# Performance work log

Measured on AMD Instinct MI355X. Metric: run time of the kernel, lower is better.

The kernel has to match this reference:

```python
import jax, jax.numpy as jnp
import numpy as np

B, N, D = 2, 2048, 1024
H, HD = 16, 64
SCALE = HD ** (-0.5)


def setup_inputs() -> dict:
    key = jax.random.key(0)
    k1, k2, k3, k4 = jax.random.split(key, 4)
    x = jax.random.normal(k1, (B, N, D), dtype=jnp.float32)
    mask = jax.random.randint(k2, (B, 1, N, N), 0, 2) == 1  # bool, True = masked out
    W_qkv = jax.random.normal(k3, (D, 3 * H * HD), dtype=jnp.float32) * (D ** -0.5)
    W_out = jax.random.normal(k4, (H * HD, D), dtype=jnp.float32) * ((H * HD) ** -0.5)
    b_out = jnp.zeros((D,), dtype=jnp.float32)
    return {"x": x, "mask": mask, "W_qkv": W_qkv, "W_out": W_out, "b_out": b_out}


def reference(x, mask, W_qkv, W_out, b_out):
    b, n, _ = x.shape
    qkv = x @ W_qkv                                  # [b, n, 3*h*hd]
    q, k, v = jnp.split(qkv, 3, axis=-1)
    split_heads = lambda t: t.reshape(b, n, H, HD).transpose(0, 2, 1, 3)  # b h n d
    q, k, v = split_heads(q), split_heads(k), split_heads(v)
    scores = jnp.einsum('bhid,bhjd->bhij', q, k) * SCALE
    scores = jnp.where(mask, jnp.finfo(scores.dtype).min, scores)
    attn = jax.nn.softmax(scores, axis=-1)           # dropout p=0 -> identity
    out = jnp.einsum('bhij,bhjd->bhid', attn, v)     # [b, h, n, hd]
    out = out.transpose(0, 2, 1, 3).reshape(b, n, H * HD)
    return out @ W_out + b_out
```

## Files before the change

### kernel.cpp

```cpp
#include <hip/hip_runtime.h>
#include <stdint.h>

typedef unsigned short u16;
typedef short short8 __attribute__((ext_vector_type(8)));
typedef float f32x4 __attribute__((ext_vector_type(4)));
typedef float f32x16 __attribute__((ext_vector_type(16)));
typedef unsigned int uint2v __attribute__((ext_vector_type(2)));

#define K2E 0.18033688011112042f

__device__ __forceinline__ u16 f2bf(float f) {
  union { float f; uint32_t u; } v;
  v.f = f;
  uint32_t u = v.u;
  u += 0x7FFFu + ((u >> 16) & 1u);
  return (u16)(u >> 16);
}

__device__ __forceinline__ uint32_t cvtpk(float lo, float hi) {
  uint32_t r;
  asm("v_cvt_pk_bf16_f32 %0, %1, %2" : "=v"(r) : "v"(lo), "v"(hi));
  return r;
}

__device__ __forceinline__ float exp2a(float x) {
  float r;
  asm("v_exp_f32 %0, %1" : "=v"(r) : "v"(x));
  return r;
}

__device__ __forceinline__ float mask_zero(float p, uint32_t zm, int oc) {
  int mext = __builtin_amdgcn_sbfe((int)zm, oc, 1);
  float r;
  asm("v_bfi_b32 %0, %1, 0, %2" : "=v"(r) : "v"(mext), "v"(p));
  return r;
}

__device__ __forceinline__ void gld_lds16(const u16* src, char* dst) {
  __builtin_amdgcn_global_load_lds((const __attribute__((address_space(1))) void*)src,
                                   (__attribute__((address_space(3))) void*)dst, 16, 0, 0);
}

__device__ __forceinline__ void pack_frags(const f32x16& v, short8& fa, short8& fb) {
  union U { uint32_t w[4]; short8 v8; };
  uint32_t X0 = cvtpk(v[0], v[1]),   X1 = cvtpk(v[2], v[3]);
  uint32_t Y0 = cvtpk(v[4], v[5]),   Y1 = cvtpk(v[6], v[7]);
  uint32_t X2 = cvtpk(v[8], v[9]),   X3 = cvtpk(v[10], v[11]);
  uint32_t Y2 = cvtpk(v[12], v[13]), Y3 = cvtpk(v[14], v[15]);
  uint2v r0 = __builtin_amdgcn_permlane32_swap(X0, Y0, false, false);
  uint2v r1 = __builtin_amdgcn_permlane32_swap(X1, Y1, false, false);
  uint2v r2 = __builtin_amdgcn_permlane32_swap(X2, Y2, false, false);
  uint2v r3 = __builtin_amdgcn_permlane32_swap(X3, Y3, false, false);
  U ua; ua.w[0] = r0.x; ua.w[1] = r1.x; ua.w[2] = r0.y; ua.w[3] = r1.y; fa = ua.v8;
  U ub; ub.w[0] = r2.x; ub.w[1] = r3.x; ub.w[2] = r2.y; ub.w[3] = r3.y; fb = ub.v8;
}

__global__ __launch_bounds__(256) void k_prep(const float* __restrict__ x,
                                              u16* __restrict__ xb,
                                              const float* __restrict__ Wqkv,
                                              u16* __restrict__ wqT,
                                              const float* __restrict__ Wout,
                                              u16* __restrict__ woT,
                                              const int* __restrict__ m,
                                              uint32_t* __restrict__ mw) {
  __shared__ float tsh[32][33];
  const int bid = blockIdx.x;
  const int t = threadIdx.x;
  if (bid < 4096) {
    int g = bid * 256 + t;
    float4 v = ((const float4*)x)[g];
    ushort4 o;
    o.x = f2bf(v.x); o.y = f2bf(v.y); o.z = f2bf(v.z); o.w = f2bf(v.w);
    ((ushort4*)xb)[g] = o;
  } else if (bid < 8192) {
    const float* src; u16* dst; int R, C, bb;
    if (bid < 7168) { src = Wqkv; dst = wqT; R = 1024; C = 3072; bb = bid - 4096;
    } else           { src = Wout; dst = woT; R = 1024; C = 1024; bb = bid - 7168; }
    const int nbx = C >> 5;
    const int c0 = (bb % nbx) * 32, r0 = (bb / nbx) * 32;
    const int tx = t & 31, ty = t >> 5;
#pragma unroll
    for (int i = 0; i < 4; ++i)
      tsh[ty + 8 * i][tx] = src[(size_t)(r0 + ty + 8 * i) * C + c0 + tx];
    __syncthreads();
#pragma unroll
    for (int i = 0; i < 4; ++i)
      dst[(size_t)(c0 + ty + 8 * i) * R + r0 + tx] = f2bf(tsh[tx][ty + 8 * i]);
  } else {
    int g = (bid - 8192) * 256 + t;
    unsigned long long bal = __ballot(m[g] != 0);
    int lane = t & 63;
    if (lane == 0) mw[g >> 5] = (uint32_t)bal;
    else if (lane == 32) mw[g >> 5] = (uint32_t)(bal >> 32);
  }
}


#define GS(U, BUF)                                                   \
  {                                                                  \
    char* dA_ = lds + (BUF) * 16384 + (w << 11);                     \
    const u16* a_ = As + ((U) << 5);                                 \
    const u16* b_ = Bs + ((U) << 5);                                 \
    gld_lds16(a_, dA_);                                              \
    gld_lds16(a_ + (K << 4), dA_ + 1024);                            \
    gld_lds16(b_, dA_ + 8192);                                       \
    gld_lds16(b_ + (K << 4), dA_ + 9216);                            \
  }

#define PH(U, BUF, DOSTAGE, VMS)                                                          \
  {                                                                                       \
    asm volatile("s_waitcnt vmcnt(" VMS ")" ::: "memory");                                \
    __builtin_amdgcn_sched_barrier(0);                                                    \
    __builtin_amdgcn_s_barrier();                                                         \
    __builtin_amdgcn_sched_barrier(0);                                                    \
    const char* rb_ = lds + (BUF) * 16384;                                                \
    short8 af[4], bfr[4];                                                                 \
    _Pragma("unroll")                                                                     \
    for (int mi = 0; mi < 4; ++mi) {                                                      \
      int row = wm * 64 + mi * 16 + lr;                                                   \
      af[mi] = *(const short8*)(rb_ + row * 64 + ((lg ^ ((row >> 1) & 3)) << 4));         \
    }                                                                                     \
    _Pragma("unroll")                                                                     \
    for (int ni = 0; ni < 4; ++ni) {                                                      \
      int row = wn * 64 + ni * 16 + lr;                                                   \
      bfr[ni] = *(const short8*)(rb_ + 8192 + row * 64 + ((lg ^ ((row >> 1) & 3)) << 4)); \
    }                                                                                     \
    asm volatile("s_waitcnt lgkmcnt(0)" ::: "memory");                                    \
    __builtin_amdgcn_sched_barrier(0);                                                    \
    __builtin_amdgcn_s_barrier();                                                        \
    __builtin_amdgcn_sched_barrier(0);                                                    \
    if (DOSTAGE) GS((U) + 3, BUF);                                                        \
    __builtin_amdgcn_s_setprio(1);                                                        \
    _Pragma("unroll")                                                                     \
    for (int mi = 0; mi < 4; ++mi)                                                        \
      _Pragma("unroll")                                                                   \
      for (int ni = 0; ni < 4; ++ni)                                                      \
        acc[mi][ni] =                                                                     \
            __builtin_amdgcn_mfma_f32_16x16x32_bf16(af[mi], bfr[ni], acc[mi][ni], 0, 0, 0); \
    __builtin_amdgcn_s_setprio(0);                                                        \
  }

__device__ __forceinline__ void gemm_core(const u16* __restrict__ A,
                                          const u16* __restrict__ Bt,
                                          int K, int m0, int n0,
                                          f32x4 (&acc)[4][4], char* lds) {
  const int t = threadIdx.x;
  const int l = t & 63;
  const int w = t >> 6;
  const int wm = w >> 1, wn = w & 1;
  const int lr = l & 15, lg = l >> 4;
  const int r0 = (w << 5) + (l >> 2);
  const int c = (l & 3) ^ ((r0 >> 1) & 3);
  const u16* As = A + (size_t)(m0 + r0) * K + c * 8;
  const u16* Bs = Bt + (size_t)(n0 + r0) * K + c * 8;

  GS(0, 0);
  GS(1, 1);
  GS(2, 2);

#pragma unroll 1
  for (int i = 0; i < 9; ++i) {
    const int u = 3 * i;
    PH(u + 0, 0, true, "8");
    PH(u + 1, 1, true, "8");
    PH(u + 2, 2, true, "8");
  }
  PH(27, 0, true, "8");
  PH(28, 1, true, "8");
  PH(29, 2, false, "8");
  PH(30, 0, false, "4");
  PH(31, 1, false, "0");
}

__global__ __launch_bounds__(256, 3) void k_gemm_qkv(const u16* __restrict__ xb,
                                                     const u16* __restrict__ wqT,
                                                     u16* __restrict__ Qb,
                                                     u16* __restrict__ Kb,
                                                     u16* __restrict__ VT) {
  __shared__ char lds[49152] __attribute__((aligned(128)));
  const int bid = blockIdx.x;
  const int wg = (bid & 7) * 96 + (bid >> 3);
  const int m0 = (wg / 24) * 128, n0 = (wg % 24) * 128;
  f32x4 acc[4][4] = {};
  gemm_core(xb, wqT, 1024, m0, n0, acc, lds);
  const int l = threadIdx.x & 63, w = threadIdx.x >> 6;
  const int wm = w >> 1, wn = w & 1;
  const int lr = l & 15, lg = l >> 4;
  const int b = m0 >> 11;
  if (n0 >= 2048) {
    __syncthreads();
    u16* lt = (u16*)lds;
#pragma unroll
    for (int mi = 0; mi < 4; ++mi)
#pragma unroll
      for (int ni = 0; ni < 4; ++ni)
#pragma unroll
        for (int r = 0; r < 4; ++r) {
          int ml = wm * 64 + mi * 16 + lg * 4 + r;
          int nl = wn * 64 + ni * 16 + lr;
          lt[nl * 136 + ml] = f2bf(acc[mi][ni][r]);
        }
    __syncthreads();
    const int nl = threadIdx.x >> 1, hf = threadIdx.x & 1;
    const int nn = n0 - 2048 + nl;
    const int seq = (m0 & 2047) + hf * 64;
    u16* dst = VT + ((size_t)((b << 4) + (nn >> 6)) * 64 + (nn & 63)) * 2048 + seq;
    const u16* srcr = lt + nl * 136 + hf * 64;
#pragma unroll
    for (int i = 0; i < 8; ++i)
      *(uint4*)(dst + i * 8) = *(const uint4*)(srcr + i * 8);
  } else {
#pragma unroll
    for (int mi = 0; mi < 4; ++mi)
#pragma unroll
      for (int ni = 0; ni < 4; ++ni)
#pragma unroll
        for (int r = 0; r < 4; ++r) {
          int m = m0 + wm * 64 + mi * 16 + lg * 4 + r;
          int n = n0 + wn * 64 + ni * 16 + lr;
          int seq = m & 2047;
          float av = acc[mi][ni][r];
          if (n < 1024) {
            Qb[((size_t)((b << 4) + (n >> 6)) * 2048 + seq) * 64 + (n & 63)] = f2bf(av * K2E);
          } else {
            int nn = n - 1024;
            Kb[((size_t)((b << 4) + (nn >> 6)) * 2048 + seq) * 64 + (nn & 63)] = f2bf(av);
          }
        }
  }
}


#define OGS(U, BUF)                                                  \
  {                                                                  \
    char* d_ = lds + (BUF) * 12288 + (w << 10);                      \
    const u16* a_ = As + ((U) << 5);                                 \
    const u16* b_ = Bs + ((U) << 5);                                 \
    gld_lds16(a_, d_);                                               \
    gld_lds16(b_, d_ + 4096);                                        \
    gld_lds16(b_ + (K << 6), d_ + 8192);                             \
  }

#define OPH(U, BUF, DOSTAGE, VMS)                                                         \
  {                                                                                       \
    asm volatile("s_waitcnt vmcnt(" VMS ")" ::: "memory");                                \
    __builtin_amdgcn_sched_barrier(0);                                                    \
    __builtin_amdgcn_s_barrier();                                                         \
    __builtin_amdgcn_sched_barrier(0);                                                    \
    const char* rb_ = lds + (BUF) * 12288;                                                \
    short8 af[2], bfr[4];                                                                 \
    _Pragma("unroll")                                                                     \
    for (int mi = 0; mi < 2; ++mi) {                                                      \
      int row = wm * 32 + mi * 16 + lr;                                                   \
      af[mi] = *(const short8*)(rb_ + row * 64 + ((lg ^ ((row >> 1) & 3)) << 4));         \
    }                                                                                     \
    _Pragma("unroll")                                                                     \
    for (int ni = 0; ni < 4; ++ni) {                                                      \
      int row = wn * 64 + ni * 16 + lr;                                                   \
      bfr[ni] = *(const short8*)(rb_ + 4096 + row * 64 + ((lg ^ ((row >> 1) & 3)) << 4)); \
    }                                                                                     \
    asm volatile("s_waitcnt lgkmcnt(0)" ::: "memory");                                    \
    __builtin_amdgcn_sched_barrier(0);                                                    \
    __builtin_amdgcn_s_barrier();                                                        \
    __builtin_amdgcn_sched_barrier(0);                                                    \
    if (DOSTAGE) OGS((U) + 3, BUF);                                                       \
    __builtin_amdgcn_s_setprio(1);                                                        \
    _Pragma("unroll")                                                                     \
    for (int mi = 0; mi < 2; ++mi)                                                        \
      _Pragma("unroll")                                                                   \
      for (int ni = 0; ni < 4; ++ni)                                                      \
        acc[mi][ni] =                                                                     \
            __builtin_amdgcn_mfma_f32_16x16x32_bf16(af[mi], bfr[ni], acc[mi][ni], 0, 0, 0); \
    __builtin_amdgcn_s_setprio(0);                                                        \
  }

__global__ __launch_bounds__(256, 4) void k_gemm_out(const u16* __restrict__ ao,
                                                     const u16* __restrict__ woT,
                                                     const float* __restrict__ bias,
                                                     float* __restrict__ out) {
  __shared__ char lds[36864] __attribute__((aligned(128)));
  const int K = 1024;
  const int bid = blockIdx.x;
  const int wg = (bid & 7) * 64 + (bid >> 3);
  const int m0 = (wg >> 3) * 64, n0 = (wg & 7) * 128;
  const int t = threadIdx.x;
  const int l = t & 63;
  const int w = t >> 6;
  const int wm = w >> 1, wn = w & 1;
  const int lr = l & 15, lg = l >> 4;
  const int sr = (w << 4) + (l >> 2);
  const int sc = (l & 3) ^ ((sr >> 1) & 3);
  const u16* As = ao + (size_t)(m0 + sr) * K + sc * 8;
  const u16* Bs = woT + (size_t)(n0 + sr) * K + sc * 8;

  f32x4 acc[2][4] = {};

  OGS(0, 0);
  OGS(1, 1);
  OGS(2, 2);

#pragma unroll 1
  for (int i = 0; i < 9; ++i) {
    const int u = 3 * i;
    OPH(u + 0, 0, true, "6");
    OPH(u + 1, 1, true, "6");
    OPH(u + 2, 2, true, "6");
  }
  OPH(27, 0, true, "6");
  OPH(28, 1, true, "6");
  OPH(29, 2, false, "6");
  OPH(30, 0, false, "3");
  OPH(31, 1, false, "0");

#pragma unroll
  for (int mi = 0; mi < 2; ++mi)
#pragma unroll
    for (int ni = 0; ni < 4; ++ni)
#pragma unroll
      for (int r = 0; r < 4; ++r) {
        int m = m0 + wm * 32 + mi * 16 + lg * 4 + r;
        int n = n0 + wn * 64 + ni * 16 + lr;
        out[(size_t)m * 1024 + n] = acc[mi][ni][r] + bias[n];
      }
}

__global__ __launch_bounds__(512, 4) void k_attn(const u16* __restrict__ Qg,
                                                 const u16* __restrict__ Kg,
                                                 const u16* __restrict__ Vg,
                                                 const uint32_t* __restrict__ maskw,
                                                 u16* __restrict__ AO) {
  __shared__ char lds[65536] __attribute__((aligned(128)));
  const int bid0 = blockIdx.x;
  const int bid = (bid0 & 7) * 64 + (bid0 >> 3);
  const int qt = bid & 15;
  const int hd = (bid >> 4) & 15;
  const int b = bid >> 8;
  const int bh = (b << 4) + hd;
  const int tx = threadIdx.x, l = tx & 63, w = tx >> 6;
  const int wq = w & 3, kvh = w >> 2;
  const int l31 = l & 31, h = l >> 5;
  const int hx4 = (h ^ (l & 7)) << 4;
  const int sc8 = ((l & 7) ^ (l >> 3)) << 3;
  const int lr8 = l >> 3;

  const u16* Qp = Qg + (size_t)bh * 131072;
  const int q = qt * 128 + wq * 32 + l31;
  const int kv0 = kvh << 10;

  const u16* kg = Kg + (size_t)bh * 131072 + (size_t)(kv0 + 16 * wq + lr8) * 64 + sc8;
  const u16* vg = Vg + (size_t)bh * 131072 + (size_t)(16 * wq + lr8) * 2048 + kv0 + sc8;
  const uint2v* mp = (const uint2v*)(maskw + ((size_t)(b << 11) + q) * 64) + (kvh << 4);

  short8 qf[4];
#pragma unroll
  for (int s = 0; s < 4; ++s)
    qf[s] = *(const short8*)(Qp + (size_t)q * 64 + s * 16 + h * 8);

  const short8 ones8 = {0x3F80, 0x3F80, 0x3F80, 0x3F80, 0x3F80, 0x3F80, 0x3F80, 0x3F80};
  f32x16 Oa[2] = {};
  f32x16 acc_l = {};
  char* ldsH = lds + (kvh << 15);

#define STAGE(BSEL, TT)                                       \
  {                                                           \
    char* base_ = ldsH + (BSEL) * 16384 + (wq << 11);         \
    const u16* k_ = kg + ((size_t)(TT) << 12);                \
    const u16* v_ = vg + ((size_t)(TT) << 6);                 \
    gld_lds16(k_, base_);                                     \
    gld_lds16(k_ + 512, base_ + 1024);                        \
    gld_lds16(v_, base_ + 8192);                              \
    gld_lds16(v_ + 16384, base_ + 9216);                      \
  }

  STAGE(0, 0);

#pragma unroll 1
  for (int tt = 0; tt < 16; ++tt) {
    __syncthreads();
    if (tt + 1 < 16) STAGE((tt + 1) & 1, tt + 1);
    const uint2v mm = mp[tt];
    const char* kbase = ldsH + (tt & 1) * 16384 + l31 * 128;
    const char* vbase = kbase + 8192;

    f32x16 sa = {}, sb = {};
    __builtin_amdgcn_s_setprio(1);
#pragma unroll
    for (int s = 0; s < 4; ++s) {
      short8 k0 = *(const short8*)(kbase + ((s << 5) ^ hx4));
      short8 k1 = *(const short8*)(kbase + 4096 + ((s << 5) ^ hx4));
      sa = __builtin_amdgcn_mfma_f32_32x32x16_bf16(k0, qf[s], sa, 0, 0, 0);
      sb = __builtin_amdgcn_mfma_f32_32x32x16_bf16(k1, qf[s], sb, 0, 0, 0);
    }
    __builtin_amdgcn_s_setprio(0);

    const uint32_t zm0 = mm.x >> (4 * h);
    const uint32_t zm1 = mm.y >> (4 * h);
#pragma unroll
    for (int r = 0; r < 16; ++r) {
      const int oc = (r & 3) + 8 * (r >> 2);
      sa[r] = mask_zero(exp2a(sa[r]), zm0, oc);
      sb[r] = mask_zero(exp2a(sb[r]), zm1, oc);
    }

    short8 pf[4];
    pack_frags(sa, pf[0], pf[1]);
    pack_frags(sb, pf[2], pf[3]);

    __builtin_amdgcn_s_setprio(1);
#pragma unroll
    for (int cc = 0; cc < 4; ++cc) {
      short8 v0 = *(const short8*)(vbase + ((cc << 5) ^ hx4));
      short8 v1 = *(const short8*)(vbase + 4096 + ((cc << 5) ^ hx4));
      Oa[0] = __builtin_amdgcn_mfma_f32_32x32x16_bf16(v0, pf[cc], Oa[0], 0, 0, 0);
      Oa[1] = __builtin_amdgcn_mfma_f32_32x32x16_bf16(v1, pf[cc], Oa[1], 0, 0, 0);
      acc_l = __builtin_amdgcn_mfma_f32_32x32x16_bf16(ones8, pf[cc], acc_l, 0, 0, 0);
    }
    __builtin_amdgcn_s_setprio(0);
  }
#undef STAGE

  __syncthreads();
  float* cb = (float*)lds;
  if (kvh) {
#pragma unroll
    for (int r = 0; r < 32; ++r)
      cb[((wq << 5) + r) * 64 + l] = Oa[r >> 4][r & 15];
    cb[8192 + (wq << 6) + l] = acc_l[0];
  }
  __syncthreads();
  if (!kvh) {
#pragma unroll
    for (int r = 0; r < 32; ++r)
      Oa[r >> 4][r & 15] += cb[((wq << 5) + r) * 64 + l];
    float lt = acc_l[0] + cb[8192 + (wq << 6) + l];
    float inv = 1.0f / fmaxf(lt, 1e-30f);
    u16* orow = AO + ((size_t)(b << 11) + q) * 1024 + hd * 64 + h * 4;
#pragma unroll
    for (int dt = 0; dt < 2; ++dt)
#pragma unroll
      for (int rq = 0; rq < 4; ++rq) {
        uint32_t w0 = cvtpk(Oa[dt][4 * rq + 0] * inv, Oa[dt][4 * rq + 1] * inv);
        uint32_t w1 = cvtpk(Oa[dt][4 * rq + 2] * inv, Oa[dt][4 * rq + 3] * inv);
        *(uint32_t*)(orow + dt * 32 + rq * 8) = w0;
        *(uint32_t*)(orow + dt * 32 + rq * 8 + 2) = w1;
      }
  }
}


extern "C" void kernel_launch(void* const* d_in, const int* in_sizes, int n_in,
                              void* d_out, int out_size, void* d_ws, size_t ws_size,
                              hipStream_t stream) {
  const float* x = (const float*)d_in[0];
  const int* mask = (const int*)d_in[1];
  const float* Wqkv = (const float*)d_in[2];
  const float* Wout = (const float*)d_in[3];
  const float* bout = (const float*)d_in[4];
  float* out = (float*)d_out;
  char* ws = (char*)d_ws;
  const size_t MB = 1u << 20;
  if (ws_size < 49 * MB) return;

  u16* xb = (u16*)(ws);
  u16* wqT = (u16*)(ws + 8 * MB);
  u16* woT = (u16*)(ws + 14 * MB);
  uint32_t* mw = (uint32_t*)(ws + 16 * MB);
  u16* Qb = (u16*)(ws + 17 * MB);
  u16* Kb = (u16*)(ws + 25 * MB);
  u16* VT = (u16*)(ws + 33 * MB);
  u16* AO = (u16*)(ws + 41 * MB);

  k_prep<<<40960, 256, 0, stream>>>(x, xb, Wqkv, wqT, Wout, woT, mask, mw);
  k_gemm_qkv<<<768, 256, 0, stream>>>(xb, wqT, Qb, Kb, VT);
  k_attn<<<512, 512, 0, stream>>>(Qb, Kb, VT, mw, AO);
  k_gemm_out<<<512, 256, 0, stream>>>(AO, woT, bout, out);
}
```

Baseline: 125.8 us.

## Fold mask bit-packing into QKV GEMM launch and reorder attention K/V staging

Mask ballot-packing moves out of the prep kernel into 2048 extra blocks appended to the QKV GEMM grid. Each of these blocks loops over 4096 mask elements, so the memory-bound mask read can overlap with the compute-bound GEMM blocks instead of running in the prep kernel beforehand. In the attention loop, the next K/V tile's global-to-LDS staging is now issued after the QK MFMAs, and the V fragments are loaded into registers before the exp/mask/pack step, to hide LDS latency. The cost is more register pressure in attention and possible interference between mask blocks and GEMM tail blocks.

```diff
diff --git a/kernel.cpp b/kernel.cpp
--- a/kernel.cpp
+++ b/kernel.cpp
@@ -60,9 +60,7 @@
                                               const float* __restrict__ Wqkv,
                                               u16* __restrict__ wqT,
                                               const float* __restrict__ Wout,
-                                              u16* __restrict__ woT,
-                                              const int* __restrict__ m,
-                                              uint32_t* __restrict__ mw) {
+                                              u16* __restrict__ woT) {
   __shared__ float tsh[32][33];
   const int bid = blockIdx.x;
   const int t = threadIdx.x;
@@ -72,7 +70,7 @@
     ushort4 o;
     o.x = f2bf(v.x); o.y = f2bf(v.y); o.z = f2bf(v.z); o.w = f2bf(v.w);
     ((ushort4*)xb)[g] = o;
-  } else if (bid < 8192) {
+  } else {
     const float* src; u16* dst; int R, C, bb;
     if (bid < 7168) { src = Wqkv; dst = wqT; R = 1024; C = 3072; bb = bid - 4096;
     } else           { src = Wout; dst = woT; R = 1024; C = 1024; bb = bid - 7168; }
@@ -86,12 +84,6 @@
 #pragma unroll
     for (int i = 0; i < 4; ++i)
       dst[(size_t)(c0 + ty + 8 * i) * R + r0 + tx] = f2bf(tsh[tx][ty + 8 * i]);
-  } else {
-    int g = (bid - 8192) * 256 + t;
-    unsigned long long bal = __ballot(m[g] != 0);
-    int lane = t & 63;
-    if (lane == 0) mw[g >> 5] = (uint32_t)bal;
-    else if (lane == 32) mw[g >> 5] = (uint32_t)(bal >> 32);
   }
 }
 
@@ -176,9 +168,23 @@
                                                      const u16* __restrict__ wqT,
                                                      u16* __restrict__ Qb,
                                                      u16* __restrict__ Kb,
-                                                     u16* __restrict__ VT) {
+                                                     u16* __restrict__ VT,
+                                                     const int* __restrict__ m,
+                                                     uint32_t* __restrict__ mw) {
   __shared__ char lds[49152] __attribute__((aligned(128)));
   const int bid = blockIdx.x;
+  if (bid >= 768) {
+    const int base = (bid - 768) * 4096;
+    const int lane = threadIdx.x & 63;
+#pragma unroll 1
+    for (int it = 0; it < 16; ++it) {
+      int g = base + it * 256 + threadIdx.x;
+      unsigned long long bal = __ballot(m[g] != 0);
+      if (lane == 0) mw[g >> 5] = (uint32_t)bal;
+      else if (lane == 32) mw[g >> 5] = (uint32_t)(bal >> 32);
+    }
+    return;
+  }
   const int wg = (bid & 7) * 96 + (bid >> 3);
   const int m0 = (wg / 24) * 128, n0 = (wg % 24) * 128;
   f32x4 acc[4][4] = {};
@@ -377,7 +383,6 @@
 #pragma unroll 1
   for (int tt = 0; tt < 16; ++tt) {
     __syncthreads();
-    if (tt + 1 < 16) STAGE((tt + 1) & 1, tt + 1);
     const uint2v mm = mp[tt];
     const char* kbase = ldsH + (tt & 1) * 16384 + l31 * 128;
     const char* vbase = kbase + 8192;
@@ -393,6 +398,14 @@
     }
     __builtin_amdgcn_s_setprio(0);
 
+    if (tt + 1 < 16) STAGE((tt + 1) & 1, tt + 1);
+    short8 vf0[4], vf1[4];
+#pragma unroll
+    for (int cc = 0; cc < 4; ++cc) {
+      vf0[cc] = *(const short8*)(vbase + ((cc << 5) ^ hx4));
+      vf1[cc] = *(const short8*)(vbase + 4096 + ((cc << 5) ^ hx4));
+    }
+
     const uint32_t zm0 = mm.x >> (4 * h);
     const uint32_t zm1 = mm.y >> (4 * h);
 #pragma unroll
@@ -409,10 +422,8 @@
     __builtin_amdgcn_s_setprio(1);
 #pragma unroll
     for (int cc = 0; cc < 4; ++cc) {
-      short8 v0 = *(const short8*)(vbase + ((cc << 5) ^ hx4));
-      short8 v1 = *(const short8*)(vbase + 4096 + ((cc << 5) ^ hx4));
-      Oa[0] = __builtin_amdgcn_mfma_f32_32x32x16_bf16(v0, pf[cc], Oa[0], 0, 0, 0);
-      Oa[1] = __builtin_amdgcn_mfma_f32_32x32x16_bf16(v1, pf[cc], Oa[1], 0, 0, 0);
+      Oa[0] = __builtin_amdgcn_mfma_f32_32x32x16_bf16(vf0[cc], pf[cc], Oa[0], 0, 0, 0);
+      Oa[1] = __builtin_amdgcn_mfma_f32_32x32x16_bf16(vf1[cc], pf[cc], Oa[1], 0, 0, 0);
       acc_l = __builtin_amdgcn_mfma_f32_32x32x16_bf16(ones8, pf[cc], acc_l, 0, 0, 0);
     }
     __builtin_amdgcn_s_setprio(0);
@@ -470,8 +481,8 @@
   u16* VT = (u16*)(ws + 33 * MB);
   u16* AO = (u16*)(ws + 41 * MB);
 
-  k_prep<<<40960, 256, 0, stream>>>(x, xb, Wqkv, wqT, Wout, woT, mask, mw);
-  k_gemm_qkv<<<768, 256, 0, stream>>>(xb, wqT, Qb, Kb, VT);
+  k_prep<<<8192, 256, 0, stream>>>(x, xb, Wqkv, wqT, Wout, woT);
+  k_gemm_qkv<<<2816, 256, 0, stream>>>(xb, wqT, Qb, Kb, VT, mask, mw);
   k_attn<<<512, 512, 0, stream>>>(Qb, Kb, VT, mw, AO);
   k_gemm_out<<<512, 256, 0, stream>>>(AO, woT, bout, out);
 }
```

Result: slower. 146.3 us (+16.3%).

## Remove KV-split in attention kernel; each block processes full KV sequence

Applied to the files above, without the earlier changes.

The attention kernel previously split the KV sequence across two groups of four waves (512 threads) and merged partial outputs and row sums through LDS. Now each block uses four waves that iterate over all 32 KV tiles, which removes the cross-wave LDS reduction and its two barriers and halves LDS use to 32KB. In exchange each block does twice as many serial iterations with half the waves, so there is less parallelism to hide latency, although lower LDS use may allow more blocks per CU.

```diff
diff --git a/kernel.cpp b/kernel.cpp
--- a/kernel.cpp
+++ b/kernel.cpp
@@ -324,20 +324,19 @@
       }
 }
 
-__global__ __launch_bounds__(512, 4) void k_attn(const u16* __restrict__ Qg,
+__global__ __launch_bounds__(256, 4) void k_attn(const u16* __restrict__ Qg,
                                                  const u16* __restrict__ Kg,
                                                  const u16* __restrict__ Vg,
                                                  const uint32_t* __restrict__ maskw,
                                                  u16* __restrict__ AO) {
-  __shared__ char lds[65536] __attribute__((aligned(128)));
+  __shared__ char lds[32768] __attribute__((aligned(128)));
   const int bid0 = blockIdx.x;
   const int bid = (bid0 & 7) * 64 + (bid0 >> 3);
   const int qt = bid & 15;
   const int hd = (bid >> 4) & 15;
   const int b = bid >> 8;
   const int bh = (b << 4) + hd;
-  const int tx = threadIdx.x, l = tx & 63, w = tx >> 6;
-  const int wq = w & 3, kvh = w >> 2;
+  const int tx = threadIdx.x, l = tx & 63, wq = tx >> 6;
   const int l31 = l & 31, h = l >> 5;
   const int hx4 = (h ^ (l & 7)) << 4;
   const int sc8 = ((l & 7) ^ (l >> 3)) << 3;
@@ -345,11 +344,10 @@
 
   const u16* Qp = Qg + (size_t)bh * 131072;
   const int q = qt * 128 + wq * 32 + l31;
-  const int kv0 = kvh << 10;
-
-  const u16* kg = Kg + (size_t)bh * 131072 + (size_t)(kv0 + 16 * wq + lr8) * 64 + sc8;
-  const u16* vg = Vg + (size_t)bh * 131072 + (size_t)(16 * wq + lr8) * 2048 + kv0 + sc8;
-  const uint2v* mp = (const uint2v*)(maskw + ((size_t)(b << 11) + q) * 64) + (kvh << 4);
+
+  const u16* kg = Kg + (size_t)bh * 131072 + (size_t)(16 * wq + lr8) * 64 + sc8;
+  const u16* vg = Vg + (size_t)bh * 131072 + (size_t)(16 * wq + lr8) * 2048 + sc8;
+  const uint2v* mp = (const uint2v*)(maskw + ((size_t)(b << 11) + q) * 64);
 
   short8 qf[4];
 #pragma unroll
@@ -359,11 +357,10 @@
   const short8 ones8 = {0x3F80, 0x3F80, 0x3F80, 0x3F80, 0x3F80, 0x3F80, 0x3F80, 0x3F80};
   f32x16 Oa[2] = {};
   f32x16 acc_l = {};
-  char* ldsH = lds + (kvh << 15);
 
 #define STAGE(BSEL, TT)                                       \
   {                                                           \
-    char* base_ = ldsH + (BSEL) * 16384 + (wq << 11);         \
+    char* base_ = lds + (BSEL) * 16384 + (wq << 11);          \
     const u16* k_ = kg + ((size_t)(TT) << 12);                \
     const u16* v_ = vg + ((size_t)(TT) << 6);                 \
     gld_lds16(k_, base_);                                     \
@@ -375,11 +372,11 @@
   STAGE(0, 0);
 
 #pragma unroll 1
-  for (int tt = 0; tt < 16; ++tt) {
+  for (int tt = 0; tt < 32; ++tt) {
     __syncthreads();
-    if (tt + 1 < 16) STAGE((tt + 1) & 1, tt + 1);
+    if (tt + 1 < 32) STAGE((tt + 1) & 1, tt + 1);
     const uint2v mm = mp[tt];
-    const char* kbase = ldsH + (tt & 1) * 16384 + l31 * 128;
+    const char* kbase = lds + (tt & 1) * 16384 + l31 * 128;
     const char* vbase = kbase + 8192;
 
     f32x16 sa = {}, sb = {};
@@ -419,32 +416,17 @@
   }
 #undef STAGE
 
-  __syncthreads();
-  float* cb = (float*)lds;
-  if (kvh) {
-#pragma unroll
-    for (int r = 0; r < 32; ++r)
-      cb[((wq << 5) + r) * 64 + l] = Oa[r >> 4][r & 15];
-    cb[8192 + (wq << 6) + l] = acc_l[0];
-  }
-  __syncthreads();
-  if (!kvh) {
-#pragma unroll
-    for (int r = 0; r < 32; ++r)
-      Oa[r >> 4][r & 15] += cb[((wq << 5) + r) * 64 + l];
-    float lt = acc_l[0] + cb[8192 + (wq << 6) + l];
-    float inv = 1.0f / fmaxf(lt, 1e-30f);
-    u16* orow = AO + ((size_t)(b << 11) + q) * 1024 + hd * 64 + h * 4;
-#pragma unroll
-    for (int dt = 0; dt < 2; ++dt)
-#pragma unroll
-      for (int rq = 0; rq < 4; ++rq) {
-        uint32_t w0 = cvtpk(Oa[dt][4 * rq + 0] * inv, Oa[dt][4 * rq + 1] * inv);
-        uint32_t w1 = cvtpk(Oa[dt][4 * rq + 2] * inv, Oa[dt][4 * rq + 3] * inv);
-        *(uint32_t*)(orow + dt * 32 + rq * 8) = w0;
-        *(uint32_t*)(orow + dt * 32 + rq * 8 + 2) = w1;
-      }
-  }
+  float inv = 1.0f / fmaxf(acc_l[0], 1e-30f);
+  u16* orow = AO + ((size_t)(b << 11) + q) * 1024 + hd * 64 + h * 4;
+#pragma unroll
+  for (int dt = 0; dt < 2; ++dt)
+#pragma unroll
+    for (int rq = 0; rq < 4; ++rq) {
+      uint32_t w0 = cvtpk(Oa[dt][4 * rq + 0] * inv, Oa[dt][4 * rq + 1] * inv);
+      uint32_t w1 = cvtpk(Oa[dt][4 * rq + 2] * inv, Oa[dt][4 * rq + 3] * inv);
+      *(uint32_t*)(orow + dt * 32 + rq * 8) = w0;
+      *(uint32_t*)(orow + dt * 32 + rq * 8 + 2) = w1;
+    }
 }
 
 
@@ -472,6 +454,6 @@
 
   k_prep<<<40960, 256, 0, stream>>>(x, xb, Wqkv, wqT, Wout, woT, mask, mw);
   k_gemm_qkv<<<768, 256, 0, stream>>>(xb, wqT, Qb, Kb, VT);
-  k_attn<<<512, 512, 0, stream>>>(Qb, Kb, VT, mw, AO);
+  k_attn<<<512, 256, 0, stream>>>(Qb, Kb, VT, mw, AO);
   k_gemm_out<<<512, 256, 0, stream>>>(AO, woT, bout, out);
 }
```

After: 126.7 us. About the same (+0.8%).
